# Kernel tuning notes

Measured on AMD Instinct MI355X. Metric: run time of the kernel, lower is better.

The kernel has to match this reference:

```python
import jax, jax.numpy as jnp
import numpy as np

MARGIN = 0.0
GAP = 0.4
N, D, C = 8192, 128, 10


def setup_inputs() -> dict:
    key = jax.random.key(0)
    k1, k2, k3 = jax.random.split(key, 3)
    inputs = jax.random.normal(k1, (N, D), dtype=jnp.float32)
    pred = jax.random.normal(k2, (N, C), dtype=jnp.float32)
    targets = jax.random.randint(k3, (N,), 0, C, dtype=jnp.int64)
    return {"inputs": inputs, "pred": pred, "targets": targets}


def reference(inputs, pred, targets):
    n = inputs.shape[0]
    # pairwise euclidean distances: ||xi||^2 + ||xj||^2 - 2 xi.xj, clamped + sqrt
    sq = jnp.sum(inputs * inputs, axis=1)                      # [n]
    dist = sq[:, None] + sq[None, :] - 2.0 * (inputs @ inputs.T)
    dist = jnp.sqrt(jnp.clip(dist, 1e-12))                     # [n, n]
    same = targets[:, None] == targets[None, :]                # [n, n] bool

    # confusion detection (original runs under no_grad)
    p = jax.nn.softmax(jax.lax.stop_gradient(pred), axis=1)
    val, top2 = jax.lax.top_k(p, 2)                            # [n,2]
    confuse = (val[:, 0] - val[:, 1] <= GAP) | (top2[:, 0] != targets)  # [n]

    # hard mining per row: hardest positive (max over same-class), hardest negative (min over diff-class)
    dist_ap = jnp.max(jnp.where(same, dist, -jnp.inf), axis=1)  # [n]
    dist_an = jnp.min(jnp.where(same, jnp.inf, dist), axis=1)   # [n]

    # MarginRankingLoss(margin=MARGIN) with y=1: mean(relu(-(an - ap) + margin)) over confused rows
    per_row = jnp.maximum(dist_ap - dist_an + MARGIN, 0.0)
    cnt = jnp.sum(confuse.astype(jnp.float32))
    loss = jnp.sum(jnp.where(confuse, per_row, 0.0)) / jnp.maximum(cnt, 1.0)
    return jnp.where(cnt > 0, loss, 0.0)
```

## Files before the change

### kernel.cpp

```cpp
#include <hip/hip_runtime.h>

#define NROWS 8192
#define DIMX  128
#define DIM2  160
#define NCLS  10
#define GAPV  0.4f
#define BIAS  2048.0f
#define C0    128.0f
#define CHUNK 512
#define SLAB  32
#define NSLAB (CHUNK / SLAB)
#define LDST  168

typedef __attribute__((ext_vector_type(8))) short bf16x8;
typedef __attribute__((ext_vector_type(4))) float f32x4;

__device__ __forceinline__ unsigned fenc(float f) {
  unsigned u = __float_as_uint(f);
  return (u & 0x80000000u) ? ~u : (u | 0x80000000u);
}
__device__ __forceinline__ float fdec(unsigned u) {
  return (u & 0x80000000u) ? __uint_as_float(u & 0x7fffffffu) : __uint_as_float(~u);
}
__device__ __forceinline__ short f2bf(float f) {
  unsigned u = __float_as_uint(f);
  u += 0x7fffu + ((u >> 16) & 1u);
  return (short)(u >> 16);
}

__global__ __launch_bounds__(256) void prep_k(const float* __restrict__ x,
                                              const int* __restrict__ tgt,
                                              const float* __restrict__ pred,
                                              short* __restrict__ xa,
                                              short* __restrict__ xbm,
                                              float* __restrict__ sq,
                                              unsigned* __restrict__ emax,
                                              unsigned* __restrict__ emin,
                                              int* __restrict__ conf) {
  const int wave = threadIdx.x >> 6;
  const int lane = threadIdx.x & 63;
  const int row  = blockIdx.x * 4 + wave;
  const float* p = x + (size_t)row * DIMX;
  const float a = p[lane];
  const float b = p[lane + 64];
  float s = a * a + b * b;
  #pragma unroll
  for (int m = 1; m < 64; m <<= 1) s += __shfl_xor(s, m, 64);

  short* pa = xa  + (size_t)row * DIM2;
  short* pb = xbm + (size_t)row * DIM2;
  pa[lane] = f2bf(a); pa[lane + 64] = f2bf(b);
  pb[lane] = f2bf(a); pb[lane + 64] = f2bf(b);

  const int cls = tgt[row];
  if (lane < 32) {
    short va, vb;
    if (lane == 0)          { va = (short)0x3F80; vb = f2bf(-0.5f * (s - C0)); }
    else if (lane <= NCLS)  { const bool hit = (lane - 1) == cls;
                              va = hit ? (short)0x4200 : (short)0;
                              vb = hit ? (short)0xC200 : (short)0; }
    else                    { va = 0; vb = 0; }
    pa[128 + lane] = va;
    pb[128 + lane] = vb;
  }

  if (lane == 0) {
    sq[row]   = s;
    emax[row] = fenc(-INFINITY);
    emin[row] = fenc(INFINITY);
    const float* pp = pred + (size_t)row * NCLS;
    float v[NCLS];
    #pragma unroll
    for (int c = 0; c < NCLS; ++c) v[c] = pp[c];
    float m1 = v[0]; int i1 = 0;
    #pragma unroll
    for (int c = 1; c < NCLS; ++c)
      if (v[c] > m1) { m1 = v[c]; i1 = c; }
    float m2 = -INFINITY, sum = 0.f;
    #pragma unroll
    for (int c = 0; c < NCLS; ++c) {
      sum += __expf(v[c] - m1);
      if (c != i1) m2 = fmaxf(m2, v[c]);
    }
    const float d01 = (1.f - __expf(m2 - m1)) / sum;
    conf[row] = (d01 <= GAPV) || (i1 != cls);
  }
}

__global__ __launch_bounds__(256, 2) void gram_k(const short* __restrict__ xa,
                                                 const short* __restrict__ xbm,
                                                 unsigned* __restrict__ emax,
                                                 unsigned* __restrict__ emin) {
  __shared__ short lds[2][SLAB * LDST];
  const int tid  = threadIdx.x;
  const int wave = tid >> 6;
  const int lane = tid & 63;
  const int quad = lane >> 4;
  const int m16  = lane & 15;
  const int i0    = blockIdx.x * 256 + wave * 64;
  const int jbase = blockIdx.y * CHUNK;

  bf16x8 A[4][5];
  #pragma unroll
  for (int r = 0; r < 4; ++r) {
    const short* pa = xa + (size_t)(i0 + r * 16 + m16) * DIM2 + quad * 8;
    #pragma unroll
    for (int ks = 0; ks < 5; ++ks)
      A[r][ks] = *(const bf16x8*)(pa + ks * 32);
  }

  float gmin[4][4], gmax[4][4];
  #pragma unroll
  for (int r = 0; r < 4; ++r)
    #pragma unroll
    for (int q = 0; q < 4; ++q) { gmin[r][q] = INFINITY; gmax[r][q] = -INFINITY; }

  const int scol = tid >> 3;
  const int sseg = tid & 3 ? (tid & 7) : (tid & 7);
  uint2 st[5];
  {
    const short* g0 = xbm + (size_t)(jbase + scol) * DIM2 + (tid & 7) * 4;
    #pragma unroll
    for (int u = 0; u < 5; ++u) st[u] = *(const uint2*)(g0 + u * 32);
  }

  for (int s = 0; s < NSLAB; ++s) {
    short* buf = lds[s & 1];
    {
      short* dst = buf + scol * LDST + (tid & 7) * 4;
      #pragma unroll
      for (int u = 0; u < 5; ++u) *(uint2*)(dst + u * 32) = st[u];
    }
    if (s + 1 < NSLAB) {
      const short* gn = xbm + (size_t)(jbase + (s + 1) * SLAB + scol) * DIM2 + (tid & 7) * 4;
      #pragma unroll
      for (int u = 0; u < 5; ++u) st[u] = *(const uint2*)(gn + u * 32);
    }
    __syncthreads();

    #pragma unroll
    for (int jt = 0; jt < SLAB / 16; ++jt) {
      const short* pb = buf + (jt * 16 + m16) * LDST + quad * 8;
      bf16x8 B[5];
      #pragma unroll
      for (int ks = 0; ks < 5; ++ks) B[ks] = *(const bf16x8*)(pb + ks * 32);

      f32x4 acc[4];
      #pragma unroll
      for (int r = 0; r < 4; ++r) acc[r] = (f32x4){0.f, 0.f, 0.f, 0.f};
      #pragma unroll
      for (int ks = 0; ks < 5; ++ks)
        #pragma unroll
        for (int r = 0; r < 4; ++r)
          acc[r] = __builtin_amdgcn_mfma_f32_16x16x32_bf16(A[r][ks], B[ks], acc[r], 0, 0, 0);

      #pragma unroll
      for (int r = 0; r < 4; ++r)
        #pragma unroll
        for (int q = 0; q < 4; ++q) {
          gmin[r][q] = fminf(gmin[r][q], acc[r][q]);
          gmax[r][q] = fmaxf(gmax[r][q], acc[r][q]);
        }
    }
  }

  #pragma unroll
  for (int m = 1; m <= 8; m <<= 1)
    #pragma unroll
    for (int r = 0; r < 4; ++r)
      #pragma unroll
      for (int q = 0; q < 4; ++q) {
        gmin[r][q] = fminf(gmin[r][q], __shfl_xor(gmin[r][q], m, 64));
        gmax[r][q] = fmaxf(gmax[r][q], __shfl_xor(gmax[r][q], m, 64));
      }

  if (m16 == 0) {
    #pragma unroll
    for (int r = 0; r < 4; ++r)
      #pragma unroll
      for (int q = 0; q < 4; ++q) {
        const int row = i0 + r * 16 + quad * 4 + q;
        atomicMax(&emax[row], fenc(C0 - 2.f * gmin[r][q] - BIAS));
        atomicMin(&emin[row], fenc(C0 - 2.f * gmax[r][q]));
      }
  }
}

__global__ __launch_bounds__(1024) void finalize_k(const float* __restrict__ sq,
                                                   const unsigned* __restrict__ emax,
                                                   const unsigned* __restrict__ emin,
                                                   const int* __restrict__ conf,
                                                   float* __restrict__ out) {
  float s = 0.f, c = 0.f;
  for (int row = threadIdx.x; row < NROWS; row += 1024) {
    if (conf[row]) {
      const float ap = sqrtf(fmaxf(sq[row] + fdec(emax[row]), 1e-12f));
      const float an = sqrtf(fmaxf(sq[row] + fdec(emin[row]), 1e-12f));
      s += fmaxf(ap - an, 0.f);
      c += 1.f;
    }
  }
  #pragma unroll
  for (int m = 1; m < 64; m <<= 1) {
    s += __shfl_xor(s, m, 64);
    c += __shfl_xor(c, m, 64);
  }
  __shared__ float ss[16], cc[16];
  const int wid = threadIdx.x >> 6;
  if ((threadIdx.x & 63) == 0) { ss[wid] = s; cc[wid] = c; }
  __syncthreads();
  if (threadIdx.x == 0) {
    float S = 0.f, C = 0.f;
    for (int w = 0; w < 16; ++w) { S += ss[w]; C += cc[w]; }
    out[0] = (C > 0.f) ? (S / fmaxf(C, 1.f)) : 0.f;
  }
}

extern "C" void kernel_launch(void* const* d_in, const int* in_sizes, int n_in,
                              void* d_out, int out_size, void* d_ws, size_t ws_size,
                              hipStream_t stream) {
  const float* x    = (const float*)d_in[0];
  const float* pred = (const float*)d_in[1];
  const int*   tgt  = (const int*)d_in[2];
  float* out = (float*)d_out;

  char* w = (char*)d_ws;
  const size_t arr_bytes = (size_t)NROWS * DIM2 * 2;
  short*    xa   = (short*)w;
  short*    xbm  = (short*)(w + arr_bytes);
  float*    sq   = (float*)(w + 2 * arr_bytes);
  unsigned* emax = (unsigned*)(w + 2 * arr_bytes + (size_t)NROWS * 4);
  unsigned* emin = (unsigned*)(w + 2 * arr_bytes + (size_t)NROWS * 8);
  int*      conf = (int*)(w + 2 * arr_bytes + (size_t)NROWS * 12);

  hipLaunchKernelGGL(prep_k, dim3(NROWS / 4), dim3(256), 0, stream,
                     x, tgt, pred, xa, xbm, sq, emax, emin, conf);
  hipLaunchKernelGGL(gram_k, dim3(NROWS / 256, NROWS / CHUNK), dim3(256), 0, stream,
                     xa, xbm, emax, emin);
  hipLaunchKernelGGL(finalize_k, dim3(1), dim3(1024), 0, stream,
                     sq, emax, emin, conf, out);
}
```

Before: 93.16 us.

## Fuse finalize into gram kernel via last-block counters and restructure slab prefetch

Removes the single-block finalize kernel by having the last column-chunk block of each row group compute that group's per-row losses. These partial sums are accumulated with global atomics, and the final block of all groups writes the output. Counters are zeroed in the prep kernel. The slab loop is also restructured: the next slab's global load is issued before the MFMA work and stored into the alternate LDS buffer afterwards, with a single barrier per iteration. The intent is to save a launch and a serial tail, at the cost of threadfence/atomic ordering complexity and a wasted wraparound load on the last slab.

Result: slower. 95.03 us (+2.0%).

```diff
diff --git a/kernel.cpp b/kernel.cpp
--- a/kernel.cpp
+++ b/kernel.cpp
@@ -8,6 +8,8 @@
 #define BIAS  2048.0f
 #define C0    128.0f
 #define CHUNK 512
+#define NCHUNK (NROWS / CHUNK)
+#define NRG    (NROWS / 256)
 #define SLAB  32
 #define NSLAB (CHUNK / SLAB)
 #define LDST  168
@@ -36,7 +38,10 @@
                                               float* __restrict__ sq,
                                               unsigned* __restrict__ emax,
                                               unsigned* __restrict__ emin,
-                                              int* __restrict__ conf) {
+                                              int* __restrict__ conf,
+                                              unsigned* __restrict__ ctrs) {
+  if (blockIdx.x == 0 && threadIdx.x < NRG + 3) ctrs[threadIdx.x] = 0u;
+
   const int wave = threadIdx.x >> 6;
   const int lane = threadIdx.x & 63;
   const int row  = blockIdx.x * 4 + wave;
@@ -89,9 +94,15 @@
 
 __global__ __launch_bounds__(256, 2) void gram_k(const short* __restrict__ xa,
                                                  const short* __restrict__ xbm,
+                                                 const float* __restrict__ sq,
+                                                 const int* __restrict__ conf,
                                                  unsigned* __restrict__ emax,
-                                                 unsigned* __restrict__ emin) {
+                                                 unsigned* __restrict__ emin,
+                                                 unsigned* __restrict__ ctrs,
+                                                 float* __restrict__ out) {
   __shared__ short lds[2][SLAB * LDST];
+  __shared__ float red[2][4];
+  __shared__ int   flag;
   const int tid  = threadIdx.x;
   const int wave = tid >> 6;
   const int lane = tid & 63;
@@ -100,6 +111,11 @@
   const int i0    = blockIdx.x * 256 + wave * 64;
   const int jbase = blockIdx.y * CHUNK;
 
+  unsigned* rg_done = ctrs;
+  unsigned* g_done  = ctrs + NRG;
+  float*    Ssum    = (float*)(ctrs + NRG + 1);
+  float*    Csum    = (float*)(ctrs + NRG + 2);
+
   bf16x8 A[4][5];
   #pragma unroll
   for (int r = 0; r < 4; ++r) {
@@ -116,28 +132,28 @@
     for (int q = 0; q < 4; ++q) { gmin[r][q] = INFINITY; gmax[r][q] = -INFINITY; }
 
   const int scol = tid >> 3;
-  const int sseg = tid & 3 ? (tid & 7) : (tid & 7);
-  uint2 st[5];
+  const int seg  = tid & 7;
+  const short* gsrc = xbm + (size_t)(jbase + scol) * DIM2 + seg * 4;
+
   {
-    const short* g0 = xbm + (size_t)(jbase + scol) * DIM2 + (tid & 7) * 4;
-    #pragma unroll
-    for (int u = 0; u < 5; ++u) st[u] = *(const uint2*)(g0 + u * 32);
-  }
-
+    uint2 st[5];
+    #pragma unroll
+    for (int u = 0; u < 5; ++u) st[u] = *(const uint2*)(gsrc + u * 32);
+    short* dst = lds[0] + scol * LDST + seg * 4;
+    #pragma unroll
+    for (int u = 0; u < 5; ++u) *(uint2*)(dst + u * 32) = st[u];
+  }
+  __syncthreads();
+
+  #pragma unroll 2
   for (int s = 0; s < NSLAB; ++s) {
-    short* buf = lds[s & 1];
-    {
-      short* dst = buf + scol * LDST + (tid & 7) * 4;
-      #pragma unroll
-      for (int u = 0; u < 5; ++u) *(uint2*)(dst + u * 32) = st[u];
-    }
-    if (s + 1 < NSLAB) {
-      const short* gn = xbm + (size_t)(jbase + (s + 1) * SLAB + scol) * DIM2 + (tid & 7) * 4;
-      #pragma unroll
-      for (int u = 0; u < 5; ++u) st[u] = *(const uint2*)(gn + u * 32);
-    }
-    __syncthreads();
-
+    const int snext = (s + 1) & (NSLAB - 1);
+    const short* gn = gsrc + (size_t)snext * SLAB * DIM2;
+    uint2 nx[5];
+    #pragma unroll
+    for (int u = 0; u < 5; ++u) nx[u] = *(const uint2*)(gn + u * 32);
+
+    const short* buf = lds[s & 1];
     #pragma unroll
     for (int jt = 0; jt < SLAB / 16; ++jt) {
       const short* pb = buf + (jt * 16 + m16) * LDST + quad * 8;
@@ -162,6 +178,11 @@
           gmax[r][q] = fmaxf(gmax[r][q], acc[r][q]);
         }
     }
+
+    short* dst = lds[(s + 1) & 1] + scol * LDST + seg * 4;
+    #pragma unroll
+    for (int u = 0; u < 5; ++u) *(uint2*)(dst + u * 32) = nx[u];
+    __syncthreads();
   }
 
   #pragma unroll
@@ -184,35 +205,43 @@
         atomicMin(&emin[row], fenc(C0 - 2.f * gmax[r][q]));
       }
   }
-}
-
-__global__ __launch_bounds__(1024) void finalize_k(const float* __restrict__ sq,
-                                                   const unsigned* __restrict__ emax,
-                                                   const unsigned* __restrict__ emin,
-                                                   const int* __restrict__ conf,
-                                                   float* __restrict__ out) {
-  float s = 0.f, c = 0.f;
-  for (int row = threadIdx.x; row < NROWS; row += 1024) {
-    if (conf[row]) {
-      const float ap = sqrtf(fmaxf(sq[row] + fdec(emax[row]), 1e-12f));
-      const float an = sqrtf(fmaxf(sq[row] + fdec(emin[row]), 1e-12f));
-      s += fmaxf(ap - an, 0.f);
-      c += 1.f;
+
+  __syncthreads();
+  if (tid == 0) {
+    __threadfence();
+    flag = (atomicAdd(&rg_done[blockIdx.x], 1u) == NCHUNK - 1u);
+  }
+  __syncthreads();
+  if (!flag) return;
+
+  const int row = blockIdx.x * 256 + tid;
+  float ps = 0.f, pc = 0.f;
+  if (conf[row]) {
+    const float hi = fdec(atomicMax(&emax[row], 0u));
+    const float lo = fdec(atomicMin(&emin[row], 0xFFFFFFFFu));
+    const float ap = sqrtf(fmaxf(sq[row] + hi, 1e-12f));
+    const float an = sqrtf(fmaxf(sq[row] + lo, 1e-12f));
+    ps = fmaxf(ap - an, 0.f);
+    pc = 1.f;
+  }
+  #pragma unroll
+  for (int m = 1; m < 64; m <<= 1) {
+    ps += __shfl_xor(ps, m, 64);
+    pc += __shfl_xor(pc, m, 64);
+  }
+  if (lane == 0) { red[0][wave] = ps; red[1][wave] = pc; }
+  __syncthreads();
+  if (tid == 0) {
+    float S = red[0][0] + red[0][1] + red[0][2] + red[0][3];
+    float C = red[1][0] + red[1][1] + red[1][2] + red[1][3];
+    atomicAdd(Ssum, S);
+    atomicAdd(Csum, C);
+    __threadfence();
+    if (atomicAdd(g_done, 1u) == NRG - 1u) {
+      const float St = atomicAdd(Ssum, 0.f);
+      const float Ct = atomicAdd(Csum, 0.f);
+      out[0] = (Ct > 0.f) ? (St / fmaxf(Ct, 1.f)) : 0.f;
     }
-  }
-  #pragma unroll
-  for (int m = 1; m < 64; m <<= 1) {
-    s += __shfl_xor(s, m, 64);
-    c += __shfl_xor(c, m, 64);
-  }
-  __shared__ float ss[16], cc[16];
-  const int wid = threadIdx.x >> 6;
-  if ((threadIdx.x & 63) == 0) { ss[wid] = s; cc[wid] = c; }
-  __syncthreads();
-  if (threadIdx.x == 0) {
-    float S = 0.f, C = 0.f;
-    for (int w = 0; w < 16; ++w) { S += ss[w]; C += cc[w]; }
-    out[0] = (C > 0.f) ? (S / fmaxf(C, 1.f)) : 0.f;
   }
 }
 
@@ -232,11 +261,10 @@
   unsigned* emax = (unsigned*)(w + 2 * arr_bytes + (size_t)NROWS * 4);
   unsigned* emin = (unsigned*)(w + 2 * arr_bytes + (size_t)NROWS * 8);
   int*      conf = (int*)(w + 2 * arr_bytes + (size_t)NROWS * 12);
+  unsigned* ctrs = (unsigned*)(w + 2 * arr_bytes + (size_t)NROWS * 16);
 
   hipLaunchKernelGGL(prep_k, dim3(NROWS / 4), dim3(256), 0, stream,
-                     x, tgt, pred, xa, xbm, sq, emax, emin, conf);
-  hipLaunchKernelGGL(gram_k, dim3(NROWS / 256, NROWS / CHUNK), dim3(256), 0, stream,
-                     xa, xbm, emax, emin);
-  hipLaunchKernelGGL(finalize_k, dim3(1), dim3(1024), 0, stream,
-                     sq, emax, emin, conf, out);
-}
+                     x, tgt, pred, xa, xbm, sq, emax, emin, conf, ctrs);
+  hipLaunchKernelGGL(gram_k, dim3(NRG, NCHUNK), dim3(256), 0, stream,
+                     xa, xbm, sq, conf, emax, emin, ctrs, out);
+}
```
